# Optimization experiments

Measured on AMD Instinct MI355X. Metric: run time of the kernel, lower is better.

## Reference

```python
import jax, jax.numpy as jnp
import numpy as np

BATCH = 512
HIDDEN_DIM = 4096
NUM_CODES = 32
CODE_DIM = 64
CODEBOOK_SIZE = 1024


def _lsa_single(cost):
    """Rectangular Hungarian (Jonker-Volgenant shortest augmenting path).
    cost: [n, m] with n <= m. Returns, for each row, the assigned column,
    minimizing total cost (matches scipy.optimize.linear_sum_assignment)."""
    n, m = cost.shape
    u = np.zeros(n + 1)
    v = np.zeros(m + 1)
    p = np.zeros(m + 1, dtype=np.int64)  # p[j]: row matched to col j (1-based); 0 = free
    for i in range(1, n + 1):
        p[0] = i
        j0 = 0
        minv = np.full(m + 1, np.inf)
        way = np.zeros(m + 1, dtype=np.int64)
        used = np.zeros(m + 1, dtype=bool)
        while True:
            used[j0] = True
            i0 = p[j0]
            free = ~used
            free[0] = False
            jfree = np.nonzero(free)[0]
            cur = cost[i0 - 1, jfree - 1] - u[i0] - v[jfree]
            upd = cur < minv[jfree]
            minv[jfree[upd]] = cur[upd]
            way[jfree[upd]] = j0
            k = jfree[np.argmin(minv[jfree])]
            delta = minv[k]
            u[p[used]] += delta
            v[used] -= delta
            minv[free] -= delta
            j0 = k
            if p[j0] == 0:
                break
        while j0 != 0:  # augment along the path
            j1 = way[j0]
            p[j0] = p[j1]
            j0 = j1
    ans = np.empty(n, dtype=np.int64)
    for j in range(1, m + 1):
        if p[j] > 0:
            ans[p[j] - 1] = j - 1
    return ans


def _lsa_batch(costs):
    costs = np.asarray(costs, dtype=np.float64)
    return np.stack([_lsa_single(c) for c in costs]).astype(np.int32)


def setup_inputs() -> dict:
    key = jax.random.key(0)
    ks = jax.random.split(key, 4)
    return {
        "x": jax.random.normal(ks[0], (BATCH, HIDDEN_DIM), jnp.float32),
        "codebook": jax.random.normal(ks[1], (CODEBOOK_SIZE, CODE_DIM), jnp.float32),
        "enc_w": jax.random.normal(ks[2], (NUM_CODES * CODE_DIM, HIDDEN_DIM), jnp.float32) * 0.02,
        "enc_b": jnp.zeros((NUM_CODES * CODE_DIM,), jnp.float32),
        "dec_w": jax.random.normal(ks[3], (HIDDEN_DIM, NUM_CODES * CODE_DIM), jnp.float32) * 0.02,
        "dec_b": jnp.zeros((HIDDEN_DIM,), jnp.float32),
    }


def reference(x, codebook, enc_w, enc_b, dec_w, dec_b):
    bs = x.shape[0]
    # encoder (torch Linear: y = x @ W.T + b)
    e = (x @ enc_w.T + enc_b).reshape(bs, NUM_CODES, CODE_DIM)
    ef = e.reshape(-1, CODE_DIM)  # [bs*num_codes, code_dim]
    # pairwise Euclidean distances to codebook entries [bs*num_codes, codebook_size]
    d2 = (jnp.sum(ef * ef, axis=1, keepdims=True)
          + jnp.sum(codebook * codebook, axis=1)
          - 2.0 * (ef @ codebook.T))
    dist = jnp.sqrt(jnp.maximum(d2, 0.0)).reshape(bs, NUM_CODES, CODEBOOK_SIZE)
    # per-sample Hungarian assignment (original uses scipy on CPU; sqrt is
    # monotone so the optimal assignment is identical)
    indices = jax.pure_callback(
        _lsa_batch,
        jax.ShapeDtypeStruct((bs, NUM_CODES), jnp.int32),
        jax.lax.stop_gradient(dist),
    )
    flat_idx = indices.reshape(-1)  # matches torch's concatenated flat indices
    q = codebook[flat_idx].reshape(bs, NUM_CODES, CODE_DIM)
    # straight-through estimator
    q_st = e + jax.lax.stop_gradient(q - e)
    r = q_st.reshape(bs, NUM_CODES * CODE_DIM) @ dec_w.T + dec_b
    return (r, q, e, flat_idx)
```

## Files before the change

### kernel.cpp

```cpp
#include <hip/hip_runtime.h>
#include <hip/hip_bf16.h>
#include <stdint.h>

#define BATCH 512
#define HID   4096
#define NC    32
#define CD    64
#define CB    1024
#define NCD   2048

typedef unsigned short u16;
typedef unsigned int   u32;
typedef __attribute__((ext_vector_type(8))) short short8;
typedef __attribute__((ext_vector_type(4))) float f32x4;

#define WAVE_SYNC()  asm volatile("s_waitcnt lgkmcnt(0)" ::: "memory")
#define SCHED_FENCE() __builtin_amdgcn_sched_barrier(0)

__device__ inline u16 bf16_rne(float f) {
  u32 u = __builtin_bit_cast(u32, f);
  u32 r = u + 0x7FFFu + ((u >> 16) & 1u);
  return (u16)(r >> 16);
}
__device__ inline float bf16_f32(u16 h) {
  u32 u = ((u32)h) << 16;
  return __builtin_bit_cast(float, u);
}
__device__ inline void split3(float a, u16& h1, u16& h2, u16& h3) {
  h1 = bf16_rne(a);
  float r1 = a - bf16_f32(h1);
  h2 = bf16_rne(r1);
  float r2 = r1 - bf16_f32(h2);
  h3 = bf16_rne(r2);
}
__device__ inline f32x4 mfma16(short8 a, short8 b, f32x4 c) {
  return __builtin_amdgcn_mfma_f32_16x16x32_bf16(a, b, c, 0, 0, 0);
}
__device__ inline void gload_lds16(const u16* g, u16* l) {
  __builtin_amdgcn_global_load_lds(
      (const __attribute__((address_space(1))) u32*)(const void*)g,
      (__attribute__((address_space(3))) u32*)(void*)l, 16, 0, 0);
}

union H8 { u16 h[8]; short8 v; };

template<int K>
__global__ __launch_bounds__(256) void conv_split3(
    const float* __restrict__ src, u16* __restrict__ d1,
    u16* __restrict__ d2, u16* __restrict__ d3) {
  __shared__ float st[4][16][36];
  const int t = threadIdx.x;
  const int wv = t >> 6, l = t & 63;
  const int g = blockIdx.x * 4 + wv;
  const int rowbase = (g / (K / 32)) * 16;
  const int kbase   = (g % (K / 32)) * 32;
  {
    const float* s = src + (size_t)(rowbase + (l >> 2)) * K + kbase + (l & 3) * 8;
    *(f32x4*)&st[wv][l >> 2][(l & 3) * 8]     = *(const f32x4*)s;
    *(f32x4*)&st[wv][l >> 2][(l & 3) * 8 + 4] = *(const f32x4*)(s + 4);
  }
  __syncthreads();
  float vv[8];
  *(f32x4*)&vv[0] = *(const f32x4*)&st[wv][l & 15][(l >> 4) * 8];
  *(f32x4*)&vv[4] = *(const f32x4*)&st[wv][l & 15][(l >> 4) * 8 + 4];
  H8 o1, o2, o3;
#pragma unroll
  for (int i = 0; i < 8; ++i) split3(vv[i], o1.h[i], o2.h[i], o3.h[i]);
  size_t off = (size_t)g * 512 + l * 8;
  *(short8*)(d1 + off) = o1.v;
  *(short8*)(d2 + off) = o2.v;
  *(short8*)(d3 + off) = o3.v;
}

template<int K>
__global__ __launch_bounds__(256) void conv_split1(
    const float* __restrict__ src, u16* __restrict__ d1) {
  __shared__ float st[4][16][36];
  const int t = threadIdx.x;
  const int wv = t >> 6, l = t & 63;
  const int g = blockIdx.x * 4 + wv;
  const int rowbase = (g / (K / 32)) * 16;
  const int kbase   = (g % (K / 32)) * 32;
  {
    const float* s = src + (size_t)(rowbase + (l >> 2)) * K + kbase + (l & 3) * 8;
    *(f32x4*)&st[wv][l >> 2][(l & 3) * 8]     = *(const f32x4*)s;
    *(f32x4*)&st[wv][l >> 2][(l & 3) * 8 + 4] = *(const f32x4*)(s + 4);
  }
  __syncthreads();
  float vv[8];
  *(f32x4*)&vv[0] = *(const f32x4*)&st[wv][l & 15][(l >> 4) * 8];
  *(f32x4*)&vv[4] = *(const f32x4*)&st[wv][l & 15][(l >> 4) * 8 + 4];
  H8 o1;
#pragma unroll
  for (int i = 0; i < 8; ++i) o1.h[i] = bf16_rne(vv[i]);
  *(short8*)(d1 + (size_t)g * 512 + l * 8) = o1.v;
}

__global__ __launch_bounds__(512) void k1_gemm(
    const float* __restrict__ A,
    const u16* __restrict__ B1, const u16* __restrict__ B2,
    const u16* __restrict__ B3, float* __restrict__ part) {
  __shared__ u16 As[2][3][8][64][8];
  __shared__ u16 Bs[2][3][8][64][8];
  const int t = threadIdx.x;
  const int wid = t >> 6, lane = t & 63;
  const int wrow = wid >> 2, wcol = wid & 3;
  const int d = blockIdx.x + (blockIdx.y << 2) + (blockIdx.z << 6);
  const int xcd = d & 7, sl = d >> 3;
  const int panel = (xcd << 3) + (sl >> 2);
  const int bm = (sl & 3) * 128;
  const int bn = (panel & 15) * 128;
  const int kz = panel >> 4;
  const int kbase = kz * 1024;
  const int arow = t >> 2;
  const int akc  = t & 3;
  const float* aptr = A + (size_t)(bm + arow) * HID + kbase + akc * 8;
  const int arf = arow >> 4;
  const int p_w = (akc << 4) | (arow & 15);
  const int s_w = p_w ^ ((p_w >> 4) & 3);
  const int s_r = lane ^ ((lane >> 4) & 3);
  const size_t nf0 = (size_t)((bn >> 4) + wid);

  f32x4 acc[4][2];
#pragma unroll
  for (int r = 0; r < 4; ++r)
#pragma unroll
    for (int c = 0; c < 2; ++c) acc[r][c] = (f32x4)0.f;

  {
    float va[8];
    *(f32x4*)&va[0] = *(const f32x4*)(aptr);
    *(f32x4*)&va[4] = *(const f32x4*)(aptr + 4);
    size_t gb = (nf0 * 128 + (size_t)(kbase >> 5)) * 512 + lane * 8;
    gload_lds16(B1 + gb, &Bs[0][0][wid][0][0]);
    gload_lds16(B2 + gb, &Bs[0][1][wid][0][0]);
    gload_lds16(B3 + gb, &Bs[0][2][wid][0][0]);
    H8 s1, s2, s3;
#pragma unroll
    for (int i = 0; i < 8; ++i) split3(va[i], s1.h[i], s2.h[i], s3.h[i]);
    *(short8*)&As[0][0][arf][s_w][0] = s1.v;
    *(short8*)&As[0][1][arf][s_w][0] = s2.v;
    *(short8*)&As[0][2][arf][s_w][0] = s3.v;
  }
  __syncthreads();

  for (int ks = 0; ks < 32; ++ks) {
    const int cur = ks & 1, nxt = cur ^ 1;
    float vb[8];
    if (ks < 31) {
      *(f32x4*)&vb[0] = *(const f32x4*)(aptr + (ks + 1) * 32);
      *(f32x4*)&vb[4] = *(const f32x4*)(aptr + (ks + 1) * 32 + 4);
      size_t gb = (nf0 * 128 + (size_t)((kbase >> 5) + ks + 1)) * 512 + lane * 8;
      gload_lds16(B1 + gb, &Bs[nxt][0][wid][0][0]);
      gload_lds16(B2 + gb, &Bs[nxt][1][wid][0][0]);
      gload_lds16(B3 + gb, &Bs[nxt][2][wid][0][0]);
    }
    short8 a0[4], a1[4], a2[4], b0[2], b1[2], b2[2];
#pragma unroll
    for (int r = 0; r < 4; ++r) {
      a0[r] = *(const short8*)&As[cur][0][wrow * 4 + r][s_r][0];
      a1[r] = *(const short8*)&As[cur][1][wrow * 4 + r][s_r][0];
      a2[r] = *(const short8*)&As[cur][2][wrow * 4 + r][s_r][0];
    }
#pragma unroll
    for (int c = 0; c < 2; ++c) {
      b0[c] = *(const short8*)&Bs[cur][0][wcol * 2 + c][lane][0];
      b1[c] = *(const short8*)&Bs[cur][1][wcol * 2 + c][lane][0];
      b2[c] = *(const short8*)&Bs[cur][2][wcol * 2 + c][lane][0];
    }
#pragma unroll
    for (int r = 0; r < 4; ++r)
#pragma unroll
      for (int c = 0; c < 2; ++c) {
        f32x4 dd = acc[r][c];
        dd = mfma16(a0[r], b0[c], dd);
        dd = mfma16(a0[r], b1[c], dd);
        dd = mfma16(a1[r], b0[c], dd);
        dd = mfma16(a1[r], b1[c], dd);
        dd = mfma16(a0[r], b2[c], dd);
        dd = mfma16(a2[r], b0[c], dd);
        acc[r][c] = dd;
      }
    if (ks < 31) {
      H8 s1, s2, s3;
#pragma unroll
      for (int i = 0; i < 8; ++i) split3(vb[i], s1.h[i], s2.h[i], s3.h[i]);
      *(short8*)&As[nxt][0][arf][s_w][0] = s1.v;
      *(short8*)&As[nxt][1][arf][s_w][0] = s2.v;
      *(short8*)&As[nxt][2][arf][s_w][0] = s3.v;
    }
    __syncthreads();
  }
  float* P = part + (size_t)kz * BATCH * NCD;
#pragma unroll
  for (int r = 0; r < 4; ++r)
#pragma unroll
    for (int c = 0; c < 2; ++c) {
      int row = bm + wrow * 64 + r * 16 + (lane >> 4) * 4;
      int col = bn + wcol * 32 + c * 16 + (lane & 15);
#pragma unroll
      for (int i = 0; i < 4; ++i)
        P[(size_t)(row + i) * NCD + col] = acc[r][c][i];
    }
}

__global__ __launch_bounds__(256) void k_reduce_bias(
    const float* __restrict__ part, const float* __restrict__ bias,
    float* __restrict__ e) {
  size_t o = ((size_t)blockIdx.x * 256 + threadIdx.x) * 4;
  int n = (int)(o & (NCD - 1));
  f32x4 s = *(const f32x4*)(part + o);
  s += *(const f32x4*)(part + (size_t)1 * BATCH * NCD + o);
  s += *(const f32x4*)(part + (size_t)2 * BATCH * NCD + o);
  s += *(const f32x4*)(part + (size_t)3 * BATCH * NCD + o);
  s += *(const f32x4*)(bias + n);
  *(f32x4*)(e + o) = s;
}

__global__ __launch_bounds__(512) void k3_gemm(
    const u16* __restrict__ Ab, const u16* __restrict__ Bb,
    const float* __restrict__ bias, float* __restrict__ C) {
  __shared__ u16 As[4][64][8];
  __shared__ u16 Bs[8][64][8];
  const int t = threadIdx.x;
  const int wid = t >> 6, lane = t & 63;
  const int wrow = wid >> 2, wcol = wid & 3;
  const int d = blockIdx.x + (blockIdx.y << 3);
  const int xcd = d & 7, sl = d >> 3;
  const int bn = ((xcd << 2) + (sl >> 3)) * 128;
  const int bm = (sl & 7) * 64;
  f32x4 acc[2][2];
#pragma unroll
  for (int r = 0; r < 2; ++r)
#pragma unroll
    for (int c = 0; c < 2; ++c) acc[r][c] = (f32x4)0.f;

  for (int ks = 0; ks < 64; ++ks) {
    {
      size_t gb = (((size_t)(bn >> 4) + wid) * 64 + ks) * 512 + lane * 8;
      gload_lds16(Bb + gb, &Bs[wid][0][0]);
      if (wid < 4) {
        size_t ga = (((size_t)(bm >> 4) + wid) * 64 + ks) * 512 + lane * 8;
        gload_lds16(Ab + ga, &As[wid][0][0]);
      }
    }
    __syncthreads();
    short8 a[2], b[2];
#pragma unroll
    for (int r = 0; r < 2; ++r) a[r] = *(const short8*)&As[wrow * 2 + r][lane][0];
#pragma unroll
    for (int c = 0; c < 2; ++c) b[c] = *(const short8*)&Bs[wcol * 2 + c][lane][0];
#pragma unroll
    for (int r = 0; r < 2; ++r)
#pragma unroll
      for (int c = 0; c < 2; ++c) acc[r][c] = mfma16(a[r], b[c], acc[r][c]);
    __syncthreads();
  }
#pragma unroll
  for (int r = 0; r < 2; ++r)
#pragma unroll
    for (int c = 0; c < 2; ++c) {
      int row = bm + wrow * 32 + r * 16 + (lane >> 4) * 4;
      int col = bn + wcol * 32 + c * 16 + (lane & 15);
      float bb = bias[col];
#pragma unroll
      for (int i = 0; i < 4; ++i)
        C[(size_t)(row + i) * HID + col] = acc[r][c][i] + bb;
    }
}

__global__ __launch_bounds__(512) void k_cost(
    const float* __restrict__ e_glob,
    const float* __restrict__ codebook,
    float* __restrict__ cost) {
  __shared__ u16 Ea[2][3][8][64][8];
  __shared__ u16 Cbs[2][3][8][64][8];
  __shared__ float enorm[128], cnorm[128];
  const int t = threadIdx.x;
  const int wid = t >> 6, lane = t & 63;
  const int wrow = wid >> 2, wcol = wid & 3;
  const int r0 = blockIdx.x * 128;
  const int c0 = blockIdx.y * 128;

  {
    const int fr = lane & 15, kc = lane >> 4;
    const float* ea = e_glob   + (size_t)(r0 + wid * 16 + fr) * CD + kc * 8;
    const float* cb = codebook + (size_t)(c0 + wid * 16 + fr) * CD + kc * 8;
#pragma unroll
    for (int ks = 0; ks < 2; ++ks) {
      float va[8], vb[8];
      *(f32x4*)&va[0] = *(const f32x4*)(ea + ks * 32);
      *(f32x4*)&va[4] = *(const f32x4*)(ea + ks * 32 + 4);
      *(f32x4*)&vb[0] = *(const f32x4*)(cb + ks * 32);
      *(f32x4*)&vb[4] = *(const f32x4*)(cb + ks * 32 + 4);
      H8 a1, a2, a3, b1, b2, b3;
#pragma unroll
      for (int i = 0; i < 8; ++i) {
        split3(va[i], a1.h[i], a2.h[i], a3.h[i]);
        split3(vb[i], b1.h[i], b2.h[i], b3.h[i]);
      }
      *(short8*)&Ea[ks][0][wid][lane][0] = a1.v;
      *(short8*)&Ea[ks][1][wid][lane][0] = a2.v;
      *(short8*)&Ea[ks][2][wid][lane][0] = a3.v;
      *(short8*)&Cbs[ks][0][wid][lane][0] = b1.v;
      *(short8*)&Cbs[ks][1][wid][lane][0] = b2.v;
      *(short8*)&Cbs[ks][2][wid][lane][0] = b3.v;
    }
  }
  if (t < 256) {
    const int which = t >> 7, idx = t & 127;
    const float* p = which ? codebook + (size_t)(c0 + idx) * CD
                           : e_glob   + (size_t)(r0 + idx) * CD;
    float s = 0.f;
#pragma unroll
    for (int k = 0; k < 16; ++k) {
      f32x4 v = *(const f32x4*)(p + k * 4);
      s += v.x * v.x + v.y * v.y + v.z * v.z + v.w * v.w;
    }
    if (which) cnorm[idx] = s; else enorm[idx] = s;
  }
  __syncthreads();

  f32x4 acc[4][2];
#pragma unroll
  for (int r = 0; r < 4; ++r)
#pragma unroll
    for (int c = 0; c < 2; ++c) acc[r][c] = (f32x4)0.f;
#pragma unroll
  for (int ks = 0; ks < 2; ++ks) {
    short8 a0[4], a1[4], a2[4], b0[2], b1[2], b2[2];
#pragma unroll
    for (int r = 0; r < 4; ++r) {
      a0[r] = *(const short8*)&Ea[ks][0][wrow * 4 + r][lane][0];
      a1[r] = *(const short8*)&Ea[ks][1][wrow * 4 + r][lane][0];
      a2[r] = *(const short8*)&Ea[ks][2][wrow * 4 + r][lane][0];
    }
#pragma unroll
    for (int c = 0; c < 2; ++c) {
      b0[c] = *(const short8*)&Cbs[ks][0][wcol * 2 + c][lane][0];
      b1[c] = *(const short8*)&Cbs[ks][1][wcol * 2 + c][lane][0];
      b2[c] = *(const short8*)&Cbs[ks][2][wcol * 2 + c][lane][0];
    }
#pragma unroll
    for (int r = 0; r < 4; ++r)
#pragma unroll
      for (int c = 0; c < 2; ++c) {
        f32x4 dd = acc[r][c];
        dd = mfma16(a0[r], b0[c], dd);
        dd = mfma16(a0[r], b1[c], dd);
        dd = mfma16(a1[r], b0[c], dd);
        dd = mfma16(a1[r], b1[c], dd);
        dd = mfma16(a0[r], b2[c], dd);
        dd = mfma16(a2[r], b0[c], dd);
        acc[r][c] = dd;
      }
  }
#pragma unroll
  for (int r = 0; r < 4; ++r)
#pragma unroll
    for (int c = 0; c < 2; ++c) {
      const int rl = wrow * 64 + r * 16 + (lane >> 4) * 4;
      const int cl = wcol * 32 + c * 16 + (lane & 15);
      const float cn = cnorm[cl];
#pragma unroll
      for (int i = 0; i < 4; ++i) {
        float d2 = enorm[rl + i] + cn - 2.f * acc[r][c][i];
        cost[(size_t)(r0 + rl + i) * CB + c0 + cl] = sqrtf(fmaxf(d2, 0.f));
      }
    }
}

__global__ __launch_bounds__(64, 1) void k_assign(
    const float* __restrict__ cost_g, const float* __restrict__ codebook,
    float* __restrict__ q_out, float* __restrict__ idx_out) {
  __shared__ int idxl[32];
  const int lane = threadIdx.x;
  const int s = blockIdx.x;
  const float* __restrict__ cost = cost_g + (size_t)s * NC * CB;

  double v_[16], minv_[16];
  u32 wp_[16];
  double u_val = 0.0;
#pragma unroll
  for (int r = 0; r < 16; ++r) { v_[r] = 0.0; wp_[r] = 0; }

  float pf[16];
#pragma unroll
  for (int r = 0; r < 16; ++r) pf[r] = cost[r * 64 + lane];

  for (int i = 1; i <= NC; ++i) {
#pragma unroll
    for (int r = 0; r < 16; ++r) minv_[r] = 1e300;
    u32 col_used = 0;
    unsigned long long rowmask = 0ull;
    int j0 = 0;
    int i0 = i;
    float cc[16];
#pragma unroll
    for (int r = 0; r < 16; ++r) cc[r] = pf[r];
    int first = 1;
    for (int guard = 0; guard < 1056; ++guard) {
      rowmask |= (1ull << i0);
      const double ui0 = __shfl(u_val, i0);
      if (first && i < NC) {
#pragma unroll
        for (int r = 0; r < 16; ++r)
          pf[r] = cost[(size_t)i * CB + r * 64 + lane];
      }
      first = 0;
      double bv = 1e301; int bj = 1 << 20;
#pragma unroll
      for (int r = 0; r < 16; ++r) {
        const int j = 1 + lane + r * 64;
        if (!((col_used >> r) & 1u)) {
          double cur = (double)cc[r] - ui0 - v_[r];
          if (cur < minv_[r]) { minv_[r] = cur; wp_[r] = (wp_[r] & 0xFFFF0000u) | (u32)j0; }
          if (minv_[r] < bv) { bv = minv_[r]; bj = j; }
        }
      }
#pragma unroll
      for (int off = 1; off < 64; off <<= 1) {
        double ov = __shfl_xor(bv, off);
        int oj = __shfl_xor(bj, off);
        if (ov < bv || (ov == bv && oj < bj)) { bv = ov; bj = oj; }
      }
      const double delta = bv;
      const int k = bj;
      const int rk = (k - 1) >> 6, kl = (k - 1) & 63;
      u32 sel = 0;
#pragma unroll
      for (int r = 0; r < 16; ++r) if (r == rk) sel = wp_[r];
      const int pmk = ((u32)__shfl((int)sel, kl)) >> 16;
      float ccn[16];
      if (pmk > 0) {
        const float* crow = cost + (size_t)(pmk - 1) * CB;
#pragma unroll
        for (int r = 0; r < 16; ++r) ccn[r] = crow[r * 64 + lane];
      }
      if ((rowmask >> lane) & 1ull) u_val += delta;
#pragma unroll
      for (int r = 0; r < 16; ++r) {
        const int j = 1 + lane + r * 64;
        if ((col_used >> r) & 1u) v_[r] -= delta;
        else {
          minv_[r] -= delta;
          if (j == k) col_used |= (1u << r);
        }
      }
      j0 = k;
      if (pmk == 0) break;
      i0 = pmk;
#pragma unroll
      for (int r = 0; r < 16; ++r) cc[r] = ccn[r];
    }
    int jj = j0;
    while (jj != 0) {
      const int rj = (jj - 1) >> 6, lj = (jj - 1) & 63;
      u32 wsel = 0;
#pragma unroll
      for (int r = 0; r < 16; ++r) if (r == rj) wsel = wp_[r];
      const int j1 = ((u32)__shfl((int)wsel, lj)) & 0xFFFFu;
      int newpm;
      if (j1 == 0) newpm = i;
      else {
        const int r1 = (j1 - 1) >> 6, l1 = (j1 - 1) & 63;
        u32 psel = 0;
#pragma unroll
        for (int r = 0; r < 16; ++r) if (r == r1) psel = wp_[r];
        newpm = ((u32)__shfl((int)psel, l1)) >> 16;
      }
#pragma unroll
      for (int r = 0; r < 16; ++r)
        if (lane == lj && r == rj) wp_[r] = (wp_[r] & 0xFFFFu) | ((u32)newpm << 16);
      jj = j1;
    }
  }

#pragma unroll
  for (int r = 0; r < 16; ++r) {
    const u32 pm = wp_[r] >> 16;
    if (pm > 0) idxl[pm - 1] = lane + r * 64;
  }
  WAVE_SYNC(); SCHED_FENCE();
  if (lane < NC) idx_out[(size_t)s * NC + lane] = (float)idxl[lane];
#pragma unroll
  for (int p = 0; p < 8; ++p) {
    int vi = p * 64 + lane;
    int r = vi >> 4, c4 = vi & 15;
    int ci = idxl[r];
    float4 qv = *(const float4*)&codebook[(size_t)ci * 64 + c4 * 4];
    *(float4*)&q_out[(size_t)s * NCD + r * 64 + c4 * 4] = qv;
  }
}

extern "C" void kernel_launch(void* const* d_in, const int* in_sizes, int n_in,
                              void* d_out, int out_size, void* d_ws, size_t ws_size,
                              hipStream_t stream) {
  (void)in_sizes; (void)n_in; (void)out_size; (void)ws_size;
  const float* x        = (const float*)d_in[0];
  const float* codebook = (const float*)d_in[1];
  const float* enc_w    = (const float*)d_in[2];
  const float* enc_b    = (const float*)d_in[3];
  const float* dec_w    = (const float*)d_in[4];
  const float* dec_b    = (const float*)d_in[5];

  float* out = (float*)d_out;
  float* r_out   = out;
  float* q_out   = out + 2097152;
  float* e_out   = out + 2097152 + 1048576;
  float* idx_out = out + 2097152 + 2097152;

  char* ws = (char*)d_ws;
  u16* B1 = (u16*)ws;
  u16* B2 = (u16*)(ws + (16u << 20));
  u16* B3 = (u16*)(ws + (32u << 20));
  float* part = (float*)(ws + (48u << 20));
  float* cost_ws = (float*)ws;
  u16* qb  = (u16*)ws;
  u16* dwb = (u16*)(ws + (2u << 20));

  conv_split3<HID><<<4096, 256, 0, stream>>>(enc_w, B1, B2, B3);
  k1_gemm<<<dim3(4, 16, 4), 512, 0, stream>>>(x, B1, B2, B3, part);
  k_reduce_bias<<<1024, 256, 0, stream>>>(part, enc_b, e_out);
  k_cost<<<dim3(128, 8), 512, 0, stream>>>(e_out, codebook, cost_ws);
  k_assign<<<BATCH, 64, 0, stream>>>(cost_ws, codebook, q_out, idx_out);
  conv_split1<NCD><<<4096, 256, 0, stream>>>(dec_w, dwb);
  conv_split1<NCD><<<512, 256, 0, stream>>>(q_out, qb);
  k3_gemm<<<dim3(8, 32), 512, 0, stream>>>(qb, dwb, dec_b, r_out);
}
```

Measured before the change: 221.0 us.

## Pre-split x into bf16 triples and restructure encoder GEMM to 4-wave 64x64 tiles

```diff
diff --git a/kernel.cpp b/kernel.cpp
--- a/kernel.cpp
+++ b/kernel.cpp
@@ -96,98 +96,73 @@
   *(short8*)(d1 + (size_t)g * 512 + l * 8) = o1.v;
 }
 
-__global__ __launch_bounds__(512) void k1_gemm(
-    const float* __restrict__ A,
+__global__ __launch_bounds__(256, 3) void k1_gemm(
+    const u16* __restrict__ A1, const u16* __restrict__ A2,
+    const u16* __restrict__ A3,
     const u16* __restrict__ B1, const u16* __restrict__ B2,
     const u16* __restrict__ B3, float* __restrict__ part) {
-  __shared__ u16 As[2][3][8][64][8];
-  __shared__ u16 Bs[2][3][8][64][8];
+  __shared__ u16 lds_all[48 * 512];
   const int t = threadIdx.x;
   const int wid = t >> 6, lane = t & 63;
-  const int wrow = wid >> 2, wcol = wid & 3;
+  const int wrow = wid >> 1, wcol = wid & 1;
   const int d = blockIdx.x + (blockIdx.y << 2) + (blockIdx.z << 6);
   const int xcd = d & 7, sl = d >> 3;
   const int panel = (xcd << 3) + (sl >> 2);
   const int bm = (sl & 3) * 128;
   const int bn = (panel & 15) * 128;
   const int kz = panel >> 4;
-  const int kbase = kz * 1024;
-  const int arow = t >> 2;
-  const int akc  = t & 3;
-  const float* aptr = A + (size_t)(bm + arow) * HID + kbase + akc * 8;
-  const int arf = arow >> 4;
-  const int p_w = (akc << 4) | (arow & 15);
-  const int s_w = p_w ^ ((p_w >> 4) & 3);
-  const int s_r = lane ^ ((lane >> 4) & 3);
-  const size_t nf0 = (size_t)((bn >> 4) + wid);
-
-  f32x4 acc[4][2];
+  const int ks0 = kz * 32;
+
+  const u16* gp[12];
+#pragma unroll
+  for (int i = 0; i < 12; ++i) {
+    const int b = wid + 4 * i;
+    const int op = b >> 3;
+    const int rf = b & 7;
+    const int rf0 = (op >= 3) ? (bn >> 4) : (bm >> 4);
+    const u16* base = (op == 0) ? A1 : (op == 1) ? A2 : (op == 2) ? A3
+                    : (op == 3) ? B1 : (op == 4) ? B2 : B3;
+    gp[i] = base + (((size_t)(rf0 + rf)) * 128 + ks0) * 512 + lane * 8;
+  }
+
+  f32x4 acc[4][4];
 #pragma unroll
   for (int r = 0; r < 4; ++r)
 #pragma unroll
-    for (int c = 0; c < 2; ++c) acc[r][c] = (f32x4)0.f;
-
-  {
-    float va[8];
-    *(f32x4*)&va[0] = *(const f32x4*)(aptr);
-    *(f32x4*)&va[4] = *(const f32x4*)(aptr + 4);
-    size_t gb = (nf0 * 128 + (size_t)(kbase >> 5)) * 512 + lane * 8;
-    gload_lds16(B1 + gb, &Bs[0][0][wid][0][0]);
-    gload_lds16(B2 + gb, &Bs[0][1][wid][0][0]);
-    gload_lds16(B3 + gb, &Bs[0][2][wid][0][0]);
-    H8 s1, s2, s3;
-#pragma unroll
-    for (int i = 0; i < 8; ++i) split3(va[i], s1.h[i], s2.h[i], s3.h[i]);
-    *(short8*)&As[0][0][arf][s_w][0] = s1.v;
-    *(short8*)&As[0][1][arf][s_w][0] = s2.v;
-    *(short8*)&As[0][2][arf][s_w][0] = s3.v;
-  }
-  __syncthreads();
+    for (int c = 0; c < 4; ++c) acc[r][c] = (f32x4)0.f;
 
   for (int ks = 0; ks < 32; ++ks) {
-    const int cur = ks & 1, nxt = cur ^ 1;
-    float vb[8];
-    if (ks < 31) {
-      *(f32x4*)&vb[0] = *(const f32x4*)(aptr + (ks + 1) * 32);
-      *(f32x4*)&vb[4] = *(const f32x4*)(aptr + (ks + 1) * 32 + 4);
-      size_t gb = (nf0 * 128 + (size_t)((kbase >> 5) + ks + 1)) * 512 + lane * 8;
-      gload_lds16(B1 + gb, &Bs[nxt][0][wid][0][0]);
-      gload_lds16(B2 + gb, &Bs[nxt][1][wid][0][0]);
-      gload_lds16(B3 + gb, &Bs[nxt][2][wid][0][0]);
-    }
-    short8 a0[4], a1[4], a2[4], b0[2], b1[2], b2[2];
+#pragma unroll
+    for (int i = 0; i < 12; ++i) {
+      gload_lds16(gp[i], &lds_all[(wid + 4 * i) * 512]);
+      gp[i] += 512;
+    }
+    __syncthreads();
+    short8 b0[4], b1[4], b2[4];
+#pragma unroll
+    for (int c = 0; c < 4; ++c) {
+      const int cf = wcol * 4 + c;
+      b0[c] = *(const short8*)&lds_all[(24 + 0 * 8 + cf) * 512 + lane * 8];
+      b1[c] = *(const short8*)&lds_all[(24 + 1 * 8 + cf) * 512 + lane * 8];
+      b2[c] = *(const short8*)&lds_all[(24 + 2 * 8 + cf) * 512 + lane * 8];
+    }
 #pragma unroll
     for (int r = 0; r < 4; ++r) {
-      a0[r] = *(const short8*)&As[cur][0][wrow * 4 + r][s_r][0];
-      a1[r] = *(const short8*)&As[cur][1][wrow * 4 + r][s_r][0];
-      a2[r] = *(const short8*)&As[cur][2][wrow * 4 + r][s_r][0];
-    }
-#pragma unroll
-    for (int c = 0; c < 2; ++c) {
-      b0[c] = *(const short8*)&Bs[cur][0][wcol * 2 + c][lane][0];
-      b1[c] = *(const short8*)&Bs[cur][1][wcol * 2 + c][lane][0];
-      b2[c] = *(const short8*)&Bs[cur][2][wcol * 2 + c][lane][0];
-    }
-#pragma unroll
-    for (int r = 0; r < 4; ++r)
-#pragma unroll
-      for (int c = 0; c < 2; ++c) {
+      const int rf = wrow * 4 + r;
+      short8 a0 = *(const short8*)&lds_all[(0 * 8 + rf) * 512 + lane * 8];
+      short8 a1 = *(const short8*)&lds_all[(1 * 8 + rf) * 512 + lane * 8];
+      short8 a2 = *(const short8*)&lds_all[(2 * 8 + rf) * 512 + lane * 8];
+#pragma unroll
+      for (int c = 0; c < 4; ++c) {
         f32x4 dd = acc[r][c];
-        dd = mfma16(a0[r], b0[c], dd);
-        dd = mfma16(a0[r], b1[c], dd);
-        dd = mfma16(a1[r], b0[c], dd);
-        dd = mfma16(a1[r], b1[c], dd);
-        dd = mfma16(a0[r], b2[c], dd);
-        dd = mfma16(a2[r], b0[c], dd);
+        dd = mfma16(a0, b0[c], dd);
+        dd = mfma16(a0, b1[c], dd);
+        dd = mfma16(a1, b0[c], dd);
+        dd = mfma16(a1, b1[c], dd);
+        dd = mfma16(a0, b2[c], dd);
+        dd = mfma16(a2, b0[c], dd);
         acc[r][c] = dd;
       }
-    if (ks < 31) {
-      H8 s1, s2, s3;
-#pragma unroll
-      for (int i = 0; i < 8; ++i) split3(vb[i], s1.h[i], s2.h[i], s3.h[i]);
-      *(short8*)&As[nxt][0][arf][s_w][0] = s1.v;
-      *(short8*)&As[nxt][1][arf][s_w][0] = s2.v;
-      *(short8*)&As[nxt][2][arf][s_w][0] = s3.v;
     }
     __syncthreads();
   }
@@ -195,9 +170,9 @@
 #pragma unroll
   for (int r = 0; r < 4; ++r)
 #pragma unroll
-    for (int c = 0; c < 2; ++c) {
+    for (int c = 0; c < 4; ++c) {
       int row = bm + wrow * 64 + r * 16 + (lane >> 4) * 4;
-      int col = bn + wcol * 32 + c * 16 + (lane & 15);
+      int col = bn + wcol * 64 + c * 16 + (lane & 15);
 #pragma unroll
       for (int i = 0; i < 4; ++i)
         P[(size_t)(row + i) * NCD + col] = acc[r][c][i];
@@ -518,9 +493,13 @@
   float* cost_ws = (float*)ws;
   u16* qb  = (u16*)ws;
   u16* dwb = (u16*)(ws + (2u << 20));
-
+  u16* A1 = (u16*)r_out;
+  u16* A2 = (u16*)r_out + 2097152;
+  u16* A3 = (u16*)q_out;
+
+  conv_split3<HID><<<1024, 256, 0, stream>>>(x, A1, A2, A3);
   conv_split3<HID><<<4096, 256, 0, stream>>>(enc_w, B1, B2, B3);
-  k1_gemm<<<dim3(4, 16, 4), 512, 0, stream>>>(x, B1, B2, B3, part);
+  k1_gemm<<<dim3(4, 16, 4), 256, 0, stream>>>(A1, A2, A3, B1, B2, B3, part);
   k_reduce_bias<<<1024, 256, 0, stream>>>(part, enc_b, e_out);
   k_cost<<<dim3(128, 8), 512, 0, stream>>>(e_out, codebook, cost_ws);
   k_assign<<<BATCH, 64, 0, stream>>>(cost_ws, codebook, q_out, idx_out);
```

Measured after the change: 222.3 us. Within noise of the previous version (+0.6%).
